# Kernel tuning notes

Hardware: AMD Instinct MI355X
Metric: run time of the kernel (lower is better)

Reference implementation:

```python
import jax, jax.numpy as jnp
import numpy as np

ALPHA, BETA, LAMDA = 1.0, 4.0, 0.0
TEMPERATURE = 4.0
WARMUP = 10
RATE = 0.93
CE_W = 1.0


def setup_inputs() -> dict:
    key = jax.random.key(0)
    k1, k2, k3 = jax.random.split(key, 3)
    B, L = 1024, 32000
    logits_student = jax.random.normal(k1, (B, L), dtype=jnp.float32)
    logits_teacher = jax.random.normal(k2, (B, L), dtype=jnp.float32)
    target = jax.random.randint(k3, (B,), 0, L, dtype=jnp.int64)
    return {"logits_student": logits_student, "logits_teacher": logits_teacher,
            "target": target, "epoch_idx": 12}


def _kl_sum(log_q, p):
    # F.kl_div(log_q, p, reduction='sum') = sum p * (log p - log_q), with 0*log0 := 0
    safe_log_p = jnp.log(jnp.where(p > 0, p, 1.0))
    return jnp.sum(jnp.where(p > 0, p * (safe_log_p - log_q), 0.0))


def _gkd_loss(ls, lt, target):
    B, L = ls.shape
    T = TEMPERATURE
    rows = jnp.arange(B)
    # scatter 999999 at the target column so target class always lands in hard set
    class_select = ls.at[rows, target].set(999999.0)
    # per-class softmax mass summed over batch
    prob_student = jax.nn.softmax(ls, axis=1).sum(axis=0)            # [L]
    sorted_prob = -jnp.sort(-prob_student)                           # descending
    cs = jnp.cumsum(sorted_prob)
    # torch loop: first idx in range(1, L, 100) with cumsum[:idx] >= rate*B
    cand = jnp.arange(1, L, 100)
    cond = cs[cand - 1] >= RATE * B
    hcm_n = cand[jnp.argmax(cond)]                                   # traced scalar
    # hard_mask[i, c] = 1 iff rank of c in row i (desc) < hcm_n
    order = jnp.argsort(-class_select, axis=1)                       # [B, L]
    take = (jnp.arange(L) < hcm_n).astype(ls.dtype)                  # [L]
    hard_mask = jnp.zeros_like(ls).at[rows[:, None], order].set(
        jnp.broadcast_to(take, (B, L)))
    hard_mask = jax.lax.stop_gradient(hard_mask)
    nhard_mask = 1.0 - hard_mask
    # binary (group) KL
    ps = jax.nn.softmax(ls / T, axis=1)
    pt = jax.nn.softmax(lt / T, axis=1)
    cat = lambda t: jnp.stack([(t * hard_mask).sum(1), (t * nhard_mask).sum(1)], axis=1)
    ps2, pt2 = cat(ps), cat(pt)
    binary_loss = _kl_sum(jnp.log(ps2), pt2) * T ** 2 / B
    # hard-group KL (mask out non-hard classes with -1000)
    pth = jax.nn.softmax(lt / T - 1000.0 * nhard_mask, axis=1)
    lsh = jax.nn.log_softmax(ls / T - 1000.0 * nhard_mask, axis=1)
    hard_loss = _kl_sum(lsh, pth) * T ** 2 / B
    # non-hard-group KL
    ptn = jax.nn.softmax(lt / T - 1000.0 * hard_mask, axis=1)
    lsn = jax.nn.log_softmax(ls / T - 1000.0 * hard_mask, axis=1)
    nhard_loss = _kl_sum(lsn, ptn) * T ** 2 / B
    return ALPHA * binary_loss + BETA * hard_loss + LAMDA * nhard_loss


def reference(logits_student, logits_teacher, target, epoch_idx):
    B = logits_student.shape[0]
    logp = jax.nn.log_softmax(logits_student, axis=1)
    loss_ce = CE_W * (-jnp.mean(logp[jnp.arange(B), target]))
    warm = min(epoch_idx / WARMUP, 1.0)
    loss_kd = warm * _gkd_loss(logits_student, logits_teacher, target)
    return (logits_student, loss_ce, loss_kd)
```

## Files before the change

### kernel.cpp

```cpp
#include <hip/hip_runtime.h>
#include <hip/hip_bf16.h>
#include <math.h>

#define BB 1024
#define LL 32000
#define NCHUNK 16
#define ROWS_PER_CHUNK (BB / NCHUNK)
#define NT 1024
#define CAP 512

#define NBUCK 16384
#define BSHIFT 18
#define QMASK ((1ull << 48) - 1)
#define K3H_NBLK (LL / 256)

constexpr float TINV = 0.25f;


typedef float vfloat4 __attribute__((ext_vector_type(4)));

__device__ __forceinline__ unsigned f2u(float x) {
  unsigned b = __float_as_uint(x);
  return (b & 0x80000000u) ? ~b : (b | 0x80000000u);
}
__device__ __forceinline__ float u2f(unsigned u) {
  unsigned b = (u & 0x80000000u) ? (u ^ 0x80000000u) : ~u;
  return __uint_as_float(b);
}
__device__ __forceinline__ float u16tof(unsigned short u16) {
  return u2f(((unsigned)u16 << 16) | 0x8000u);
}

__global__ __launch_bounds__(256) void k1_stats(
    const float* __restrict__ ls, const int* __restrict__ tgt,
    float* __restrict__ stats) {
  int r = blockIdx.x, tid = threadIdx.x;
  int lane = tid & 63, wv = tid >> 6;
  const float4* a4 = (const float4*)(ls + (size_t)r * LL);
  float s1 = 0.f, sT = 0.f;
  for (int i = tid; i < LL / 4; i += 256) {
    float4 a = a4[i];
    s1 += __expf(a.x) + __expf(a.y) + __expf(a.z) + __expf(a.w);
    sT += __expf(a.x * TINV) + __expf(a.y * TINV) +
          __expf(a.z * TINV) + __expf(a.w * TINV);
  }
  for (int o = 32; o > 0; o >>= 1) {
    s1 += __shfl_down(s1, o);
    sT += __shfl_down(sT, o);
  }
  __shared__ float wsum[8];
  if (lane == 0) { wsum[wv * 2] = s1; wsum[wv * 2 + 1] = sT; }
  __syncthreads();
  if (tid == 0) {
    float t1 = wsum[0] + wsum[2] + wsum[4] + wsum[6];
    float tT = wsum[1] + wsum[3] + wsum[5] + wsum[7];
    float lst = ls[(size_t)r * LL + tgt[r]];
    float* st = stats + r * 8;
    st[0] = t1; st[1] = tT; st[2] = lst; st[3] = 1.0f / t1;
  }
}

__global__ __launch_bounds__(256) void k2a_prob_part(
    const float* __restrict__ ls, const float* __restrict__ stats,
    float* __restrict__ part, unsigned long long* __restrict__ buckets) {
  int lin = blockIdx.y * gridDim.x + blockIdx.x;
  if (threadIdx.x < 9) {
    int z = lin * 9 + threadIdx.x;
    if (z < NBUCK) buckets[z] = 0ull;
  }
  int c = blockIdx.x * 256 + threadIdx.x;
  int r0 = blockIdx.y * ROWS_PER_CHUNK;
  float acc = 0.f;
#pragma unroll 8
  for (int rr = 0; rr < ROWS_PER_CHUNK; ++rr) {
    int r = r0 + rr;
    float rs = stats[r * 8 + 3];
    acc += __expf(ls[(size_t)r * LL + c]) * rs;
  }
  part[(size_t)blockIdx.y * LL + c] = acc;
}

__global__ __launch_bounds__(256) void k3h_bucket(
    const float* __restrict__ part, unsigned long long* __restrict__ buckets) {
  __shared__ unsigned long long lh[NBUCK];
  int tid = threadIdx.x;
  for (int i = tid; i < NBUCK; i += 256) lh[i] = 0ull;
  __syncthreads();
  int e = blockIdx.x * 256 + tid;
  float acc = 0.f;
#pragma unroll
  for (int j = 0; j < NCHUNK; ++j) acc += part[(size_t)j * LL + e];
  unsigned long long q = (unsigned long long)(acc * 1048576.0f);
  atomicAdd(&lh[f2u(acc) >> BSHIFT], (1ull << 48) | q);
  __syncthreads();
  for (int i = tid; i < NBUCK; i += 256) {
    unsigned long long v = lh[i];
    if (v) atomicAdd(&buckets[i], v);
  }
}

__global__ __launch_bounds__(256) void k3h_scan(
    const unsigned long long* __restrict__ buckets, int* __restrict__ hcm) {
  __shared__ unsigned long long ps[256];
  __shared__ int bmin[256];
  int tid = threadIdx.x;
  const int CHUNK = NBUCK / 256;
  int base = tid * CHUNK;
  unsigned long long tot = 0;
  for (int i = 0; i < CHUNK; ++i)
    tot += buckets[(NBUCK - 1) - (base + i)];
  ps[tid] = tot;
  __syncthreads();
  for (int o = 1; o < 256; o <<= 1) {
    unsigned long long v = ps[tid];
    unsigned long long add = (tid >= o) ? ps[tid - o] : 0ull;
    __syncthreads();
    ps[tid] = v + add;
    __syncthreads();
  }
  unsigned long long run = (tid == 0) ? 0ull : ps[tid - 1];
  const float Rqf = 0.93f * 1024.0f * 1048576.0f;
  int best = 0x7fffffff;
  for (int i = 0; i < CHUNK; ++i) {
    unsigned long long v = buckets[(NBUCK - 1) - (base + i)];
    int cb = (int)(v >> 48);
    if (cb > 0) {
      int C = (int)(run >> 48);
      float S = (float)(run & QMASK);
      int c1 = (C / 100) * 100 + 1;
      if (c1 <= C) c1 += 100;
      int cmax = C + cb; if (cmax > 31901) cmax = 31901;
      if (c1 <= cmax) {
        float avg = (float)(v & QMASK) / (float)cb;
        for (int cand = c1; cand <= cmax; cand += 100) {
          float est = S + (float)(cand - C) * avg;
          if (est >= Rqf) { best = cand; break; }
        }
        if (best != 0x7fffffff) break;
      }
    }
    run += v;
  }
  bmin[tid] = best;
  __syncthreads();
  for (int o = 128; o > 0; o >>= 1) {
    if (tid < o) bmin[tid] = min(bmin[tid], bmin[tid + o]);
    __syncthreads();
  }
  if (tid == 0) *hcm = (bmin[0] == 0x7fffffff) ? 1 : bmin[0];
}

__global__ __launch_bounds__(1024) void k45_fused(
    const float* __restrict__ ls, const float* __restrict__ lt,
    const int* __restrict__ tgt, const int* __restrict__ hcm,
    const float* __restrict__ stats, float* __restrict__ outc,
    float* __restrict__ ce_a, float* __restrict__ bin_a,
    float* __restrict__ hd_a) {
  __shared__ unsigned short u16row[LL];
  __shared__ unsigned hist[2048];
  __shared__ unsigned scratch[1024];
  __shared__ int ctl[8];
  __shared__ float sst[8];

  int r = blockIdx.x, tid = threadIdx.x;
  int lane = tid & 63, wv = tid >> 6;
  int t = tgt[r];
  int k = *hcm;
  const float* row_s = ls + (size_t)r * LL;
  const float* row_t = lt + (size_t)r * LL;
  const unsigned U999 = f2u(999999.0f);

  for (int i = tid; i < 2048; i += NT) hist[i] = 0;
  if (tid == 0) { ctl[4] = 0; ctl[5] = 0; ctl[6] = 0; }
  if (tid < 4) sst[tid] = stats[r * 8 + tid];
  __syncthreads();

  const vfloat4* a4 = (const vfloat4*)row_s;
  vfloat4* o4 = (vfloat4*)(outc + (size_t)r * LL);
  for (int i = tid; i < LL / 4; i += NT) {
    vfloat4 a = a4[i];
    __builtin_nontemporal_store(a, &o4[i]);
    int c0 = 4 * i;
    ushort4 pk;
    unsigned short* pp = (unsigned short*)&pk;
#pragma unroll
    for (int j = 0; j < 4; ++j) {
      unsigned u = f2u(a[j]);
      pp[j] = (unsigned short)(u >> 16);
      atomicAdd(&hist[u >> 21], 1u);
    }
    *(ushort4*)(u16row + c0) = pk;
  }
  __syncthreads();
  if (tid == 0) {
    unsigned uo = f2u(row_s[t]);
    atomicAdd(&hist[uo >> 21], 0xFFFFFFFFu);
    atomicAdd(&hist[U999 >> 21], 1u);
    u16row[t] = (unsigned short)(U999 >> 16);
  }
  __syncthreads();

  {
    int* wtot = (int*)scratch;
    int h0 = (int)hist[2 * tid], h1 = (int)hist[2 * tid + 1];
    int s = h0 + h1;
    for (int o = 1; o < 64; o <<= 1) {
      int v = __shfl_down(s, o);
      if (lane + o < 64) s += v;
    }
    if (lane == 0) wtot[wv] = s;
    __syncthreads();
    int sw = 0;
    for (int w2 = wv + 1; w2 < 16; ++w2) sw += wtot[w2];
    int S_pair = s + sw;
    int i1 = S_pair - h0;
    int i2 = i1 - h1;
    if (S_pair >= k && i1 < k) { ctl[0] = 2 * tid; ctl[1] = k - i1; }
    if (i1 >= k && i2 < k) { ctl[0] = 2 * tid + 1; ctl[1] = k - i2; }
  }
  __syncthreads();
  int B11 = ctl[0], r11 = ctl[1];
  if (tid < 32) hist[tid] = 0;
  __syncthreads();

  for (int i = tid; i < LL / 4; i += NT) {
    ushort4 kk = *(const ushort4*)(u16row + 4 * i);
    const unsigned short* kp = (const unsigned short*)&kk;
#pragma unroll
    for (int j = 0; j < 4; ++j) {
      unsigned v = kp[j];
      if ((int)(v >> 5) == B11) atomicAdd(&hist[v & 31u], 1u);
    }
  }
  __syncthreads();
  if (wv == 0 && lane < 32) {
    int h = (int)hist[lane];
    int s = h;
    for (int o = 1; o < 32; o <<= 1) {
      int v = __shfl_down(s, o);
      if (lane + o < 32) s += v;
    }
    int nxt = s - h;
    if (s >= r11 && nxt < r11) { ctl[2] = lane; ctl[3] = r11 - nxt; }
  }
  __syncthreads();
  unsigned P16 = ((unsigned)B11 << 5) | (unsigned)ctl[2];
  int rr = ctl[3];

  unsigned* grp = scratch;
  for (int i = tid; i < LL / 4; i += NT) {
    ushort4 kk = *(const ushort4*)(u16row + 4 * i);
    const unsigned short* kp = (const unsigned short*)&kk;
#pragma unroll
    for (int j = 0; j < 4; ++j) {
      int c = 4 * i + j;
      if ((unsigned)kp[j] == P16) {
        int pos = atomicAdd(&ctl[4], 1);
        if (pos < CAP) {
          float x = (c == t) ? 999999.0f : row_s[c];
          grp[2 * pos] = f2u(x);
          grp[2 * pos + 1] = (unsigned)c;
        }
      }
    }
  }
  __syncthreads();
  int m = ctl[4]; if (m > CAP) m = CAP;

  for (int gi = tid; gi < m; gi += NT) {
    unsigned ui = grp[2 * gi], ci = grp[2 * gi + 1];
    int rank = 0;
    for (int j = 0; j < m; ++j) {
      unsigned uj = grp[2 * j], cj = grp[2 * j + 1];
      rank += (uj > ui || (uj == ui && cj < ci)) ? 1 : 0;
    }
    if (rank == rr - 1) { ctl[5] = (int)ci; ctl[6] = (int)ui; }
  }
  __syncthreads();
  unsigned thrU = (unsigned)ctl[6];
  int cut = ctl[5];
  unsigned short thr16 = (unsigned short)(thrU >> 16);
  __syncthreads();

  float s1 = sst[0], sT = sst[1], lst = sst[2];
  float a_s = 0.f, tT = 0.f, a_t = 0.f, w = 0.f;
  const vfloat4* b4 = (const vfloat4*)row_t;
  for (int i = tid; i < LL / 4; i += NT) {
    vfloat4 b = __builtin_nontemporal_load(&b4[i]);
    ushort4 kk = *(const ushort4*)(u16row + 4 * i);
    const unsigned short* kp = (const unsigned short*)&kk;
    int c0 = 4 * i;
#pragma unroll
    for (int j = 0; j < 4; ++j) {
      int c = c0 + j;
      float y = b[j];
      unsigned short u16 = kp[j];
      bool istgt = (c == t);
      bool hard;
      float x;
      if (u16 != thr16) {
        hard = (u16 > thr16);
        x = istgt ? lst : u16tof(u16);
      } else {
        float xe = row_s[c];
        x = istgt ? lst : xe;
        unsigned u = istgt ? U999 : f2u(xe);
        hard = (u > thrU) || (u == thrU && c <= cut);
      }
      float et = __expf(y * TINV);
      float es = __expf(x * TINV);
      tT += et;
      float h = hard ? 1.f : 0.f;
      a_t += h * et;
      w += h * et * (y - x);
      a_s += h * es;
    }
  }
  for (int o = 32; o > 0; o >>= 1) {
    a_s += __shfl_down(a_s, o);
    tT += __shfl_down(tT, o);
    a_t += __shfl_down(a_t, o);
    w += __shfl_down(w, o);
  }
  float* pf = (float*)scratch;
  if (lane == 0) {
    pf[wv * 4 + 0] = a_s; pf[wv * 4 + 1] = tT;
    pf[wv * 4 + 2] = a_t; pf[wv * 4 + 3] = w;
  }
  __syncthreads();
  if (wv == 0) {
    float aS = 0.f, t2T = 0.f, a2T = 0.f, w2w = 0.f;
    if (lane < 16) {
      aS = pf[lane * 4 + 0]; t2T = pf[lane * 4 + 1];
      a2T = pf[lane * 4 + 2]; w2w = pf[lane * 4 + 3];
    }
    for (int o = 1; o < 16; o <<= 1) {
      float sb = __shfl_down(aS, o);
      float tb = __shfl_down(t2T, o);
      float ab = __shfl_down(a2T, o);
      float wb = __shfl_down(w2w, o);
      if (lane + o < 16) { aS += sb; t2T += tb; a2T += ab; w2w += wb; }
    }
    if (lane == 0) {
      float hs = aS / sT, ht = a2T / t2T;
      float bin = 0.f;
      if (ht > 0.f) bin += ht * (logf(ht) - logf(hs));
      float htn = 1.f - ht, hsn = 1.f - hs;
      if (htn > 0.f) bin += htn * (logf(htn) - logf(hsn));
      float hd = (w2w * TINV) / a2T - logf(a2T) + logf(aS);
      ce_a[r] = logf(s1) - lst;
      bin_a[r] = bin;
      hd_a[r] = hd;
    }
  }
}

__global__ __launch_bounds__(256) void k6_final(
    const float* __restrict__ ce_a, const float* __restrict__ bin_a,
    const float* __restrict__ hd_a, const int* __restrict__ epoch,
    float* __restrict__ out2) {
  __shared__ float r1[256], r2[256], r3[256];
  int tid = threadIdx.x;
  float a = 0.f, b = 0.f, c = 0.f;
  for (int i = tid; i < BB; i += 256) { a += ce_a[i]; b += bin_a[i]; c += hd_a[i]; }
  r1[tid] = a; r2[tid] = b; r3[tid] = c;
  __syncthreads();
  for (int o = 128; o > 0; o >>= 1) {
    if (tid < o) { r1[tid] += r1[tid + o]; r2[tid] += r2[tid + o]; r3[tid] += r3[tid + o]; }
    __syncthreads();
  }
  if (tid == 0) {
    float loss_ce = r1[0] / (float)BB;
    float tsq = 16.0f / (float)BB;
    float binary_loss = r2[0] * tsq;
    float hard_loss = r3[0] * tsq;
    float warm = fminf((float)(*epoch) / 10.0f, 1.0f);
    float loss_kd = warm * (1.0f * binary_loss + 4.0f * hard_loss);
    out2[0] = loss_ce;
    out2[1] = loss_kd;
  }
}

extern "C" void kernel_launch(void* const* d_in, const int* in_sizes, int n_in,
                              void* d_out, int out_size, void* d_ws, size_t ws_size,
                              hipStream_t stream) {
  const float* ls = (const float*)d_in[0];
  const float* lt = (const float*)d_in[1];
  const int* tgt = (const int*)d_in[2];
  const int* epoch = (const int*)d_in[3];
  float* out = (float*)d_out;

  char* ws = (char*)d_ws;
  size_t off = 0;
  float* stats = (float*)(ws + off); off += (size_t)BB * 8 * 4;
  float* part = (float*)(ws + off); off += (size_t)NCHUNK * LL * 4;
  int* hcm = (int*)(ws + off); off += 256;
  float* ce_a = (float*)(ws + off); off += (size_t)BB * 4;
  float* bin_a = (float*)(ws + off); off += (size_t)BB * 4;
  float* hd_a = (float*)(ws + off); off += (size_t)BB * 4;
  unsigned long long* buckets = (unsigned long long*)(ws + off); off += (size_t)NBUCK * 8;

  hipLaunchKernelGGL(k1_stats, dim3(BB), dim3(256), 0, stream, ls, tgt, stats);
  hipLaunchKernelGGL(k2a_prob_part, dim3(LL / 256, NCHUNK), dim3(256), 0, stream, ls, stats, part, buckets);
  hipLaunchKernelGGL(k3h_bucket, dim3(K3H_NBLK), dim3(256), 0, stream, part, buckets);
  hipLaunchKernelGGL(k3h_scan, dim3(1), dim3(256), 0, stream, buckets, hcm);
  hipLaunchKernelGGL(k45_fused, dim3(BB), dim3(NT), 0, stream, ls, lt, tgt, hcm, stats, out, ce_a, bin_a, hd_a);
  hipLaunchKernelGGL(k6_final, dim3(1), dim3(256), 0, stream, ce_a, bin_a, hd_a, epoch, out + (size_t)BB * LL);
}
```

Baseline: 171.1 us.

## Fuse bucket scan into histogram kernel via last-block pattern with occupancy bitmap

```diff
diff --git a/kernel.cpp b/kernel.cpp
--- a/kernel.cpp
+++ b/kernel.cpp
@@ -4,7 +4,7 @@
 
 #define BB 1024
 #define LL 32000
-#define NCHUNK 16
+#define NCHUNK 8
 #define ROWS_PER_CHUNK (BB / NCHUNK)
 #define NT 1024
 #define CAP 512
@@ -13,6 +13,8 @@
 #define BSHIFT 18
 #define QMASK ((1ull << 48) - 1)
 #define K3H_NBLK (LL / 256)
+#define NWORD (NBUCK / 64)
+#define MFAST 4096
 
 constexpr float TINV = 0.25f;
 
@@ -62,11 +64,15 @@
 
 __global__ __launch_bounds__(256) void k2a_prob_part(
     const float* __restrict__ ls, const float* __restrict__ stats,
-    float* __restrict__ part, unsigned long long* __restrict__ buckets) {
+    float* __restrict__ part, unsigned long long* __restrict__ buckets,
+    unsigned long long* __restrict__ aux) {
   int lin = blockIdx.y * gridDim.x + blockIdx.x;
-  if (threadIdx.x < 9) {
-    int z = lin * 9 + threadIdx.x;
+  if (threadIdx.x < 17) {
+    int z = lin * 17 + threadIdx.x;
     if (z < NBUCK) buckets[z] = 0ull;
+  }
+  if (lin == 0) {
+    for (int i = threadIdx.x; i < 1 + NWORD; i += 256) aux[i] = 0ull;
   }
   int c = blockIdx.x * 256 + threadIdx.x;
   int r0 = blockIdx.y * ROWS_PER_CHUNK;
@@ -81,8 +87,11 @@
 }
 
 __global__ __launch_bounds__(256) void k3h_bucket(
-    const float* __restrict__ part, unsigned long long* __restrict__ buckets) {
+    const float* __restrict__ part, unsigned long long* __restrict__ buckets,
+    unsigned long long* __restrict__ aux, int* __restrict__ hcm) {
   __shared__ unsigned long long lh[NBUCK];
+  __shared__ int lastf;
+  __shared__ int shm[8];
   int tid = threadIdx.x;
   for (int i = tid; i < NBUCK; i += 256) lh[i] = 0ull;
   __syncthreads();
@@ -95,36 +104,72 @@
   __syncthreads();
   for (int i = tid; i < NBUCK; i += 256) {
     unsigned long long v = lh[i];
-    if (v) atomicAdd(&buckets[i], v);
-  }
-}
-
-__global__ __launch_bounds__(256) void k3h_scan(
-    const unsigned long long* __restrict__ buckets, int* __restrict__ hcm) {
-  __shared__ unsigned long long ps[256];
-  __shared__ int bmin[256];
-  int tid = threadIdx.x;
-  const int CHUNK = NBUCK / 256;
-  int base = tid * CHUNK;
-  unsigned long long tot = 0;
-  for (int i = 0; i < CHUNK; ++i)
-    tot += buckets[(NBUCK - 1) - (base + i)];
-  ps[tid] = tot;
-  __syncthreads();
-  for (int o = 1; o < 256; o <<= 1) {
-    unsigned long long v = ps[tid];
-    unsigned long long add = (tid >= o) ? ps[tid - o] : 0ull;
-    __syncthreads();
-    ps[tid] = v + add;
-    __syncthreads();
-  }
-  unsigned long long run = (tid == 0) ? 0ull : ps[tid - 1];
+    if (v) {
+      atomicAdd(&buckets[i], v);
+      atomicOr(&aux[1 + (i >> 6)], 1ull << (i & 63));
+    }
+  }
+  __threadfence();
+  __syncthreads();
+  if (tid == 0) {
+    unsigned long long prev = atomicAdd(&aux[0], 1ull);
+    lastf = (prev == (unsigned long long)(K3H_NBLK - 1)) ? 1 : 0;
+  }
+  __syncthreads();
+  if (!lastf) return;
+
+  int* cntw = (int*)lh;
+  int* offw = cntw + 256;
+  int* binlist = offw + 256;
+  unsigned long long* vals =
+      (unsigned long long*)(binlist + MFAST);
+  unsigned long long* partials = vals + MFAST;
+
+  unsigned long long w = atomicAdd(&aux[1 + tid], 0ull);
+  cntw[tid] = __popcll(w);
+  __syncthreads();
+  {
+    int lane = tid & 63, wv = tid >> 6;
+    int s = cntw[tid];
+    for (int o = 1; o < 64; o <<= 1) {
+      int v = __shfl_down(s, o);
+      if (lane + o < 64) s += v;
+    }
+    if (lane == 0) shm[wv] = s;
+    __syncthreads();
+    int sw = 0;
+    for (int w2 = wv + 1; w2 < 4; ++w2) sw += shm[w2];
+    offw[tid] = s + sw - cntw[tid];
+  }
+  __syncthreads();
+  int m = offw[0] + cntw[0];
   const float Rqf = 0.93f * 1024.0f * 1048576.0f;
-  int best = 0x7fffffff;
-  for (int i = 0; i < CHUNK; ++i) {
-    unsigned long long v = buckets[(NBUCK - 1) - (base + i)];
-    int cb = (int)(v >> 48);
-    if (cb > 0) {
+  if (m <= MFAST) {
+    int pos = offw[tid];
+    for (int b = 63; b >= 0; --b)
+      if ((w >> b) & 1ull) binlist[pos++] = tid * 64 + b;
+    __syncthreads();
+    for (int j = tid; j < m; j += 256)
+      vals[j] = atomicAdd(&buckets[binlist[j]], 0ull);
+    __syncthreads();
+    int ck = (m + 255) / 256;
+    int j0 = tid * ck, j1 = min(m, j0 + ck);
+    unsigned long long tot = 0;
+    for (int j = j0; j < j1; ++j) tot += vals[j];
+    partials[tid] = tot;
+    __syncthreads();
+    for (int o = 1; o < 256; o <<= 1) {
+      unsigned long long v = partials[tid];
+      unsigned long long add = (tid >= o) ? partials[tid - o] : 0ull;
+      __syncthreads();
+      partials[tid] = v + add;
+      __syncthreads();
+    }
+    unsigned long long run = (tid == 0) ? 0ull : partials[tid - 1];
+    int best = 0x7fffffff;
+    for (int j = j0; j < j1; ++j) {
+      unsigned long long v = vals[j];
+      int cb = (int)(v >> 48);
       int C = (int)(run >> 48);
       float S = (float)(run & QMASK);
       int c1 = (C / 100) * 100 + 1;
@@ -138,16 +183,40 @@
         }
         if (best != 0x7fffffff) break;
       }
-    }
-    run += v;
-  }
-  bmin[tid] = best;
-  __syncthreads();
-  for (int o = 128; o > 0; o >>= 1) {
-    if (tid < o) bmin[tid] = min(bmin[tid], bmin[tid + o]);
-    __syncthreads();
-  }
-  if (tid == 0) *hcm = (bmin[0] == 0x7fffffff) ? 1 : bmin[0];
+      run += v;
+    }
+    __syncthreads();
+    cntw[tid] = best;
+    __syncthreads();
+    for (int o = 128; o > 0; o >>= 1) {
+      if (tid < o) cntw[tid] = min(cntw[tid], cntw[tid + o]);
+      __syncthreads();
+    }
+    if (tid == 0) *hcm = (cntw[0] == 0x7fffffff) ? 1 : cntw[0];
+  } else if (tid == 0) {
+    unsigned long long run = 0;
+    int best = 0x7fffffff;
+    for (int b = NBUCK - 1; b >= 0 && best == 0x7fffffff; --b) {
+      unsigned long long v = atomicAdd(&buckets[b], 0ull);
+      int cb = (int)(v >> 48);
+      if (cb > 0) {
+        int C = (int)(run >> 48);
+        float S = (float)(run & QMASK);
+        int c1 = (C / 100) * 100 + 1;
+        if (c1 <= C) c1 += 100;
+        int cmax = C + cb; if (cmax > 31901) cmax = 31901;
+        if (c1 <= cmax) {
+          float avg = (float)(v & QMASK) / (float)cb;
+          for (int cand = c1; cand <= cmax; cand += 100) {
+            float est = S + (float)(cand - C) * avg;
+            if (est >= Rqf) { best = cand; break; }
+          }
+        }
+      }
+      run += v;
+    }
+    *hcm = (best == 0x7fffffff) ? 1 : best;
+  }
 }
 
 __global__ __launch_bounds__(1024) void k45_fused(
@@ -399,11 +468,11 @@
   float* bin_a = (float*)(ws + off); off += (size_t)BB * 4;
   float* hd_a = (float*)(ws + off); off += (size_t)BB * 4;
   unsigned long long* buckets = (unsigned long long*)(ws + off); off += (size_t)NBUCK * 8;
+  unsigned long long* aux = (unsigned long long*)(ws + off); off += (size_t)(1 + NWORD) * 8;
 
   hipLaunchKernelGGL(k1_stats, dim3(BB), dim3(256), 0, stream, ls, tgt, stats);
-  hipLaunchKernelGGL(k2a_prob_part, dim3(LL / 256, NCHUNK), dim3(256), 0, stream, ls, stats, part, buckets);
-  hipLaunchKernelGGL(k3h_bucket, dim3(K3H_NBLK), dim3(256), 0, stream, part, buckets);
-  hipLaunchKernelGGL(k3h_scan, dim3(1), dim3(256), 0, stream, buckets, hcm);
+  hipLaunchKernelGGL(k2a_prob_part, dim3(LL / 256, NCHUNK), dim3(256), 0, stream, ls, stats, part, buckets, aux);
+  hipLaunchKernelGGL(k3h_bucket, dim3(K3H_NBLK), dim3(256), 0, stream, part, buckets, aux, hcm);
   hipLaunchKernelGGL(k45_fused, dim3(BB), dim3(NT), 0, stream, ls, lt, tgt, hcm, stats, out, ce_a, bin_a, hd_a);
   hipLaunchKernelGGL(k6_final, dim3(1), dim3(256), 0, stream, ce_a, bin_a, hd_a, epoch, out + (size_t)BB * LL);
 }
```

Result: faster. 163.7 us (median of 2 runs) (-4.4%).
